# Kernel optimization log

Hardware: AMD Instinct MI355X
Metric: run time of the kernel (lower is better)

The kernel has to match this reference:

```python
import jax, jax.numpy as jnp
import numpy as np

B, T, FEATS, HEAD = 2, 2048, 2048, 16
DIM_HEAD = FEATS // HEAD
EPS = float(jnp.finfo(jnp.float32).eps)  # torch nn.RMSNorm default eps=None -> dtype eps


def _rms_norm(u, g):
    # u: [..., d]; torch RMSNorm: u / sqrt(mean(u^2) + eps) * g
    return u * jax.lax.rsqrt(jnp.mean(u * u, axis=-1, keepdims=True) + EPS) * g


def setup_inputs() -> dict:
    key = jax.random.key(0)
    kx, kw = jax.random.split(key)
    x = jax.random.normal(kx, (B, T, FEATS), dtype=jnp.float32)
    W = jax.random.normal(kw, (FEATS, FEATS), dtype=jnp.float32) / np.sqrt(FEATS)
    g1 = jnp.ones((DIM_HEAD,), dtype=jnp.float32)
    g2 = jnp.ones((DIM_HEAD,), dtype=jnp.float32)
    g3 = jnp.ones((DIM_HEAD,), dtype=jnp.float32)
    return {"x": x, "W": W, "g1": g1, "g2": g2, "g3": g3}


def reference(x, W, g1, g2, g3):
    Bb, Tt, C = x.shape
    sqrt_d = jnp.asarray(DIM_HEAD ** 0.5, dtype=x.dtype)
    # tied QKV projection: torch Linear -> x @ W.T ; then split heads -> [B,H,T,D]
    w = (x @ W.T).reshape(Bb, Tt, HEAD, DIM_HEAD).transpose(0, 2, 1, 3)
    q = _rms_norm(w, g1)
    k = _rms_norm(w, g2)
    v = _rms_norm(w, g3)
    att = jnp.einsum("bhid,bhjd->bhij", q, k) / sqrt_d  # [B,H,T,T]
    # symmetric row + column softmax
    score = jax.nn.softmax(att, axis=-1) + jax.nn.softmax(att, axis=-2)
    y = jnp.einsum("bhij,bhjd->bihd", score, v).reshape(Bb, Tt, C)
    # F.linear(y, W.t()) == y @ W  (tied-weight reprojection)
    return y @ W
```

## Files before the change

kernel.cpp:

```cpp
#include <hip/hip_runtime.h>
#include <stdint.h>

#define T_SEQ 2048
#define B_SZ 2
#define N_HEAD 16
#define D_HEAD 128
#define C_DIM 2048
#define M_ROWS (B_SZ*T_SEQ)
#define N_BH (B_SZ*N_HEAD)

typedef _Float16 f16;
typedef f16 f16x8 __attribute__((ext_vector_type(8)));
typedef f16 f16x4 __attribute__((ext_vector_type(4)));
typedef float f32x4 __attribute__((ext_vector_type(4)));

#define MFMA_F16(a,b,c) __builtin_amdgcn_mfma_f32_16x16x32_f16(a,b,c,0,0,0)

#define BAR_LGKM() do { asm volatile("s_waitcnt lgkmcnt(0)" ::: "memory"); \
                        __builtin_amdgcn_s_barrier(); } while (0)
#define BAR_ALL()  do { asm volatile("s_waitcnt vmcnt(0) lgkmcnt(0)" ::: "memory"); \
                        __builtin_amdgcn_s_barrier(); } while (0)

__device__ __forceinline__ float fexp2(float x) {
#if __has_builtin(__builtin_amdgcn_exp2f)
  return __builtin_amdgcn_exp2f(x);
#else
  float r; asm("v_exp_f32 %0, %1" : "=v"(r) : "v"(x)); return r;
#endif
}

__device__ __forceinline__ void gl_lds16(const void* g, void* l) {
  __builtin_amdgcn_global_load_lds(
      (const __attribute__((address_space(1))) unsigned int*)g,
      (__attribute__((address_space(3))) unsigned int*)l, 16, 0, 0);
}

#define MB_SCALE 0.12752924444069595f
#define RMS_EPS  1.1920928955078125e-07f

__global__ void k_prep(const float* __restrict__ W, const float* __restrict__ x,
                       f16* __restrict__ Wb, f16* __restrict__ Wtb,
                       f16* __restrict__ xb) {
  __shared__ float tile[64][65];
  const int lin = blockIdx.x;
  const int t = threadIdx.x;
  if (lin < 1024) {
    const int bx = (lin & 31) * 64;
    const int by = (lin >> 5) * 64;
    const int tc = t & 63, tr4 = t >> 6;
    for (int rr = tr4; rr < 64; rr += 4) {
      float v = W[(size_t)(by + rr) * C_DIM + bx + tc];
      tile[rr][tc] = v;
      Wb[(size_t)(by + rr) * C_DIM + bx + tc] = (f16)v;
    }
    __syncthreads();
    for (int rr = tr4; rr < 64; rr += 4) {
      Wtb[(size_t)(bx + rr) * C_DIM + by + tc] = (f16)tile[tc][rr];
    }
  } else {
    int i = (lin - 1024) * 256 + t;
    const int stride = 2048 * 256;
    const int n4 = (M_ROWS * C_DIM) / 4;
    for (; i < n4; i += stride) {
      f32x4 v = ((const f32x4*)x)[i];
      f16x4 o; o[0]=(f16)v[0]; o[1]=(f16)v[1]; o[2]=(f16)v[2]; o[3]=(f16)v[3];
      ((f16x4*)xb)[i] = o;
    }
  }
}

template<typename OT>
__global__ __launch_bounds__(256, 2)
void k_gemm_bt(const f16* __restrict__ A, const f16* __restrict__ Bm,
               OT* __restrict__ C, int Nd, int Kd) {
  __shared__ __align__(16) f16 As[2][128 * 64];
  __shared__ __align__(16) f16 Bs[2][128 * 64];
  const int tid = threadIdx.x;
  const int lane = tid & 63, wid = tid >> 6;
  const int lr = lane & 15, lkg = lane >> 4;
  const int wr = wid >> 1, wc = wid & 1;
  const int tm = blockIdx.y * 128, tn = blockIdx.x * 128;

  f32x4 acc[4][4];
#pragma unroll
  for (int i = 0; i < 4; ++i)
#pragma unroll
    for (int j = 0; j < 4; ++j) acc[i][j] = (f32x4){0.f, 0.f, 0.f, 0.f};

  const int nkt = Kd >> 6;

  auto stage = [&](int buf, int kt) {
    const int k0 = kt << 6;
    for (int s = 0; s < 4; ++s) {
      const int r0 = (wid * 4 + s) * 8;
      const int r = r0 + (lane >> 3);
      const int lg = ((lane & 7) ^ (r & 7)) << 3;
      gl_lds16(A + (size_t)(tm + r) * Kd + k0 + lg, &As[buf][r0 * 64]);
      gl_lds16(Bm + (size_t)(tn + r) * Kd + k0 + lg, &Bs[buf][r0 * 64]);
    }
  };

  stage(0, 0);
  int cur = 0;
  for (int kt = 0; kt < nkt; ++kt) {
    __syncthreads();
    if (kt + 1 < nkt) stage(cur ^ 1, kt + 1);
#pragma unroll
    for (int kk = 0; kk < 2; ++kk) {
      f16x8 a[4], b[4];
#pragma unroll
      for (int i = 0; i < 4; ++i) {
        const int ra = wr * 64 + i * 16 + lr;
        const int ga = ((kk * 4 + lkg) ^ (ra & 7)) << 3;
        a[i] = *(const f16x8*)&As[cur][ra * 64 + ga];
        const int rb = wc * 64 + i * 16 + lr;
        const int gb = ((kk * 4 + lkg) ^ (rb & 7)) << 3;
        b[i] = *(const f16x8*)&Bs[cur][rb * 64 + gb];
      }
#pragma unroll
      for (int i = 0; i < 4; ++i)
#pragma unroll
        for (int j = 0; j < 4; ++j) acc[i][j] = MFMA_F16(a[i], b[j], acc[i][j]);
    }
    cur ^= 1;
  }
#pragma unroll
  for (int i = 0; i < 4; ++i) {
    const int row0 = tm + wr * 64 + i * 16 + lkg * 4;
#pragma unroll
    for (int j = 0; j < 4; ++j) {
      const int col = tn + wc * 64 + j * 16 + lr;
#pragma unroll
      for (int r = 0; r < 4; ++r)
        C[(size_t)(row0 + r) * Nd + col] = (OT)acc[i][j][r];
    }
  }
}

__global__ __launch_bounds__(256, 2)
void k_gemm_qkv(const f16* __restrict__ A, const f16* __restrict__ Bm,
                const float* __restrict__ g1, const float* __restrict__ g2,
                f16* __restrict__ nb, f16* __restrict__ mb,
                f16* __restrict__ nT) {
  __shared__ __align__(16) char smem[70656];
  f16 (*As)[128 * 64] = (f16(*)[128 * 64])smem;
  f16 (*Bs)[128 * 64] = (f16(*)[128 * 64])(smem + 32768);
  f16* Cs = (f16*)smem;
  float* sc = (float*)(smem + 69632);

  const int tid = threadIdx.x;
  const int lane = tid & 63, wid = tid >> 6;
  const int lr = lane & 15, lkg = lane >> 4;
  const int wr = wid >> 1, wc = wid & 1;
  const int tm = blockIdx.y * 128;
  const int hh = blockIdx.x;
  const int tn = hh * 128;

  f32x4 acc[4][4];
#pragma unroll
  for (int i = 0; i < 4; ++i)
#pragma unroll
    for (int j = 0; j < 4; ++j) acc[i][j] = (f32x4){0.f, 0.f, 0.f, 0.f};

  auto stage = [&](int buf, int kt) {
    const int k0 = kt << 6;
    for (int s = 0; s < 4; ++s) {
      const int r0 = (wid * 4 + s) * 8;
      const int r = r0 + (lane >> 3);
      const int lg = ((lane & 7) ^ (r & 7)) << 3;
      gl_lds16(A + (size_t)(tm + r) * C_DIM + k0 + lg, &As[buf][r0 * 64]);
      gl_lds16(Bm + (size_t)(tn + r) * C_DIM + k0 + lg, &Bs[buf][r0 * 64]);
    }
  };

  stage(0, 0);
  int cur = 0;
  for (int kt = 0; kt < 32; ++kt) {
    __syncthreads();
    if (kt + 1 < 32) stage(cur ^ 1, kt + 1);
#pragma unroll
    for (int kk = 0; kk < 2; ++kk) {
      f16x8 a[4], b[4];
#pragma unroll
      for (int i = 0; i < 4; ++i) {
        const int ra = wr * 64 + i * 16 + lr;
        const int ga = ((kk * 4 + lkg) ^ (ra & 7)) << 3;
        a[i] = *(const f16x8*)&As[cur][ra * 64 + ga];
        const int rb = wc * 64 + i * 16 + lr;
        const int gb = ((kk * 4 + lkg) ^ (rb & 7)) << 3;
        b[i] = *(const f16x8*)&Bs[cur][rb * 64 + gb];
      }
#pragma unroll
      for (int i = 0; i < 4; ++i)
#pragma unroll
        for (int j = 0; j < 4; ++j) acc[i][j] = MFMA_F16(a[i], b[j], acc[i][j]);
    }
    cur ^= 1;
  }
  __syncthreads();

#pragma unroll
  for (int i = 0; i < 4; ++i)
#pragma unroll
    for (int j = 0; j < 4; ++j)
#pragma unroll
      for (int r = 0; r < 4; ++r)
        Cs[(wr * 64 + i * 16 + lkg * 4 + r) * 136 + wc * 64 + j * 16 + lr] =
            (f16)acc[i][j][r];
  __syncthreads();

  const int row = tid >> 1, dh = tid & 1;
  f16x8 v[8];
  float ss = 0.f;
#pragma unroll
  for (int c = 0; c < 8; ++c) {
    v[c] = *(const f16x8*)&Cs[row * 136 + dh * 64 + c * 8];
#pragma unroll
    for (int e = 0; e < 8; ++e) { float f = (float)v[c][e]; ss += f * f; }
  }
  ss += __shfl_xor(ss, 1);
  const float scale = rsqrtf(ss * (1.f / 128.f) + RMS_EPS);
  if (dh == 0) sc[row] = scale;

  const int grow = tm + row;
  const int b = grow >> 11, ts = grow & (T_SEQ - 1);
  const size_t nbase =
      ((size_t)((b * N_HEAD + hh) * T_SEQ + ts)) * 128 + dh * 64;
#pragma unroll
  for (int c = 0; c < 8; ++c) {
    const int d0 = dh * 64 + c * 8;
    f16x8 n8, m8;
#pragma unroll
    for (int e = 0; e < 8; ++e) {
      const float nf = (float)v[c][e] * scale;
      n8[e] = (f16)nf;
      m8[e] = (f16)(nf * g1[d0 + e] * g2[d0 + e] * MB_SCALE);
    }
    *(f16x8*)&nb[nbase + c * 8] = n8;
    *(f16x8*)&mb[nbase + c * 8] = m8;
  }
  __syncthreads();

  const int dcol = tid >> 1, th = tid & 1;
  const size_t tbase =
      ((size_t)((b * N_HEAD + hh) * 128 + dcol)) * T_SEQ + (tm & (T_SEQ - 1)) +
      th * 64;
#pragma unroll
  for (int rr = 0; rr < 8; ++rr) {
    f16x8 o;
#pragma unroll
    for (int e = 0; e < 8; ++e) {
      const int trow = th * 64 + rr * 8 + e;
      o[e] = (f16)((float)Cs[trow * 136 + dcol] * sc[trow]);
    }
    *(f16x8*)&nT[tbase + rr * 8] = o;
  }
}

__global__ __launch_bounds__(256, 3)
void k_stats_tri(const f16* __restrict__ mIn, const f16* __restrict__ nIn,
                 float* __restrict__ Ssum) {
  __shared__ __align__(16) f16 Ns[128 * 128];
  __shared__ float redR[256];
  __shared__ float redC[256];
  const int tid = threadIdx.x, lane = tid & 63, wid = tid >> 6;
  const int lr = lane & 15, lkg = lane >> 4;
  const int wr = wid >> 1, wc = wid & 1;
  int p = blockIdx.x, it = 0, rowlen = 16;
  while (p >= rowlen) { p -= rowlen; ++it; --rowlen; }
  const int jt = it + p;
  const int bh = blockIdx.y;
  const f16* mp = mIn + (size_t)bh * T_SEQ * 128;
  const f16* np = nIn + (size_t)bh * T_SEQ * 128;

  f16x8 msr[4][4];
#pragma unroll
  for (int i = 0; i < 4; ++i)
#pragma unroll
    for (int kk = 0; kk < 4; ++kk)
      msr[i][kk] = *(const f16x8*)&mp[(size_t)(it * 128 + wr * 64 + i * 16 + lr) * 128 +
                                      (kk * 4 + lkg) * 8];

#pragma unroll
  for (int s = 0; s < 8; ++s) {
    const int r0 = (wid * 8 + s) * 4;
    const int r = r0 + (lane >> 4);
    const int lg = ((lane & 15) ^ (r & 7)) << 3;
    gl_lds16(np + (size_t)(jt * 128 + r) * 128 + lg, &Ns[r0 * 128]);
  }
  BAR_ALL();

  f32x4 acc[4][4];
#pragma unroll
  for (int i = 0; i < 4; ++i)
#pragma unroll
    for (int j = 0; j < 4; ++j) acc[i][j] = (f32x4){0.f, 0.f, 0.f, 0.f};
#pragma unroll
  for (int kk = 0; kk < 4; ++kk) {
    f16x8 b[4];
#pragma unroll
    for (int j = 0; j < 4; ++j) {
      const int rb = wc * 64 + j * 16 + lr;
      const int gb = ((kk * 4 + lkg) ^ (rb & 7)) << 3;
      b[j] = *(const f16x8*)&Ns[rb * 128 + gb];
    }
#pragma unroll
    for (int i = 0; i < 4; ++i)
#pragma unroll
      for (int j = 0; j < 4; ++j)
        acc[i][j] = MFMA_F16(msr[i][kk], b[j], acc[i][j]);
  }

  float rsum[16], csum[4];
#pragma unroll
  for (int q = 0; q < 16; ++q) rsum[q] = 0.f;
#pragma unroll
  for (int j = 0; j < 4; ++j) csum[j] = 0.f;
#pragma unroll
  for (int i = 0; i < 4; ++i)
#pragma unroll
    for (int j = 0; j < 4; ++j)
#pragma unroll
      for (int r = 0; r < 4; ++r) {
        const float e = fexp2(acc[i][j][r]);
        rsum[i * 4 + r] += e;
        csum[j] += e;
      }
#pragma unroll
  for (int q = 0; q < 16; ++q) {
    float v = rsum[q];
    v += __shfl_xor(v, 1); v += __shfl_xor(v, 2);
    v += __shfl_xor(v, 4); v += __shfl_xor(v, 8);
    rsum[q] = v;
  }
  if (lr == 0) {
#pragma unroll
    for (int q = 0; q < 16; ++q) {
      const int row = wr * 64 + (q >> 2) * 16 + lkg * 4 + (q & 3);
      redR[row * 2 + wc] = rsum[q];
    }
  }
#pragma unroll
  for (int j = 0; j < 4; ++j) {
    float v = csum[j];
    v += __shfl_xor(v, 16); v += __shfl_xor(v, 32);
    csum[j] = v;
  }
  if (lkg == 0) {
#pragma unroll
    for (int j = 0; j < 4; ++j) {
      const int col = wc * 64 + j * 16 + lr;
      redC[col * 2 + wr] = csum[j];
    }
  }
  __syncthreads();
  if (tid < 128) {
    const float rS = redR[tid * 2] + redR[tid * 2 + 1];
    atomicAdd(&Ssum[(size_t)bh * T_SEQ + it * 128 + tid], rS);
    if (it != jt) {
      const float cS = redC[tid * 2] + redC[tid * 2 + 1];
      atomicAdd(&Ssum[(size_t)bh * T_SEQ + jt * 128 + tid], cS);
    }
  }
}

__global__ void k_inv(const float* __restrict__ S, float* __restrict__ alpha) {
  const int i = blockIdx.x * blockDim.x + threadIdx.x;
  f32x4 s = ((const f32x4*)S)[i];
  f32x4 a;
#pragma unroll
  for (int e = 0; e < 4; ++e) a[e] = 1.f / s[e];
  ((f32x4*)alpha)[i] = a;
}

__global__ __launch_bounds__(256, 2)
void k_apply(const f16* __restrict__ mIn, const f16* __restrict__ nIn,
             const f16* __restrict__ nTIn, const float* __restrict__ alpha,
             const float* __restrict__ g3, f16* __restrict__ yb) {
  __shared__ __align__(16) f16 Ns[2][64 * 128];
  __shared__ __align__(16) f16 Nts[2][128 * 64];
  __shared__ __align__(16) f16 Ps[128 * 64];
  const int tid = threadIdx.x, lane = tid & 63, wid = tid >> 6;
  const int lr = lane & 15, lkg = lane >> 4;
  const int wj = wid >> 1;
  const int wi = wid & 1;
  const int lin = blockIdx.x + (blockIdx.y << 4);
  const int swz = ((lin & 7) << 6) + (lin >> 3);
  const int it = swz & 15, bh = swz >> 4;
  const int b = bh >> 4, hh = bh & 15;
  const f16* mp = mIn + (size_t)bh * T_SEQ * 128;
  const f16* np = nIn + (size_t)bh * T_SEQ * 128;
  const f16* ntp = nTIn + (size_t)bh * 128 * T_SEQ;
  const float* al = alpha + (size_t)bh * T_SEQ;

  f16x8 msr[4][4];
#pragma unroll
  for (int ii = 0; ii < 4; ++ii)
#pragma unroll
    for (int kk = 0; kk < 4; ++kk)
      msr[ii][kk] = *(const f16x8*)&mp[(size_t)(it * 128 + wi * 64 + ii * 16 + lr) * 128 +
                                       (kk * 4 + lkg) * 8];

  auto stageN = [&](int buf, int jt) {
#pragma unroll
    for (int s = 0; s < 4; ++s) {
      const int r0 = (wid * 4 + s) * 4;
      const int r = r0 + (lane >> 4);
      const int lg = ((lane & 15) ^ (r & 7)) << 3;
      gl_lds16(np + (size_t)(jt * 64 + r) * 128 + lg, &Ns[buf][r0 * 128]);
    }
  };
  auto stageNT = [&](int buf, int jt) {
#pragma unroll
    for (int s = 0; s < 4; ++s) {
      const int r0 = (wid * 4 + s) * 8;
      const int r = r0 + (lane >> 3);
      const int lg = ((lane & 7) ^ (r & 7)) << 3;
      gl_lds16(ntp + (size_t)r * T_SEQ + jt * 64 + lg, &Nts[buf][r0 * 64]);
    }
  };

  float ai[4];
#pragma unroll
  for (int ii = 0; ii < 4; ++ii) ai[ii] = al[it * 128 + wi * 64 + ii * 16 + lr];

  f32x4 yacc[4][4];
#pragma unroll
  for (int i = 0; i < 4; ++i)
#pragma unroll
    for (int j = 0; j < 4; ++j) yacc[i][j] = (f32x4){0.f, 0.f, 0.f, 0.f};

  stageN(0, 0);
  stageNT(0, 0);
  BAR_ALL();
  int cur = 0;
  for (int jt = 0; jt < 32; ++jt) {
    float aj[8];
#pragma unroll
    for (int jj = 0; jj < 2; ++jj)
#pragma unroll
      for (int r = 0; r < 4; ++r)
        aj[jj * 4 + r] = al[jt * 64 + wj * 32 + jj * 16 + lkg * 4 + r];
    if (jt < 31) { stageN(cur ^ 1, jt + 1); stageNT(cur ^ 1, jt + 1); }

    f32x4 acc[2][4];
#pragma unroll
    for (int i = 0; i < 2; ++i)
#pragma unroll
      for (int j = 0; j < 4; ++j) acc[i][j] = (f32x4){0.f, 0.f, 0.f, 0.f};
#pragma unroll
    for (int kk = 0; kk < 4; ++kk) {
      f16x8 a[2];
#pragma unroll
      for (int jj = 0; jj < 2; ++jj) {
        const int jrow = wj * 32 + jj * 16 + lr;
        a[jj] = *(const f16x8*)&Ns[cur][jrow * 128 + (((kk * 4 + lkg) ^ (jrow & 7)) << 3)];
      }
#pragma unroll
      for (int jj = 0; jj < 2; ++jj)
#pragma unroll
        for (int ii = 0; ii < 4; ++ii)
          acc[jj][ii] = MFMA_F16(a[jj], msr[ii][kk], acc[jj][ii]);
    }

#pragma unroll
    for (int jj = 0; jj < 2; ++jj)
#pragma unroll
      for (int ii = 0; ii < 4; ++ii) {
        f16x4 o;
#pragma unroll
        for (int r = 0; r < 4; ++r) {
          const float p = fexp2(acc[jj][ii][r]) * (ai[ii] + aj[jj * 4 + r]);
          o[r] = (f16)p;
        }
        const int il = wi * 64 + ii * 16 + lr;
        const int jl = wj * 32 + jj * 16 + lkg * 4;
        *(f16x4*)&Ps[il * 64 + (((jl >> 3) ^ (il & 7)) << 3) + (jl & 7)] = o;
      }
    BAR_LGKM();

#pragma unroll
    for (int kk = 0; kk < 2; ++kk) {
      f16x8 a[4], bfr[4];
#pragma unroll
      for (int dd = 0; dd < 4; ++dd) {
        const int drow = wj * 64 + dd * 16 + lr;
        a[dd] = *(const f16x8*)&Nts[cur][drow * 64 + (((kk * 4 + lkg) ^ (drow & 7)) << 3)];
      }
#pragma unroll
      for (int ii = 0; ii < 4; ++ii) {
        const int irow = wi * 64 + ii * 16 + lr;
        bfr[ii] = *(const f16x8*)&Ps[irow * 64 + (((kk * 4 + lkg) ^ (irow & 7)) << 3)];
      }
#pragma unroll
      for (int dd = 0; dd < 4; ++dd)
#pragma unroll
        for (int ii = 0; ii < 4; ++ii)
          yacc[dd][ii] = MFMA_F16(a[dd], bfr[ii], yacc[dd][ii]);
    }
    BAR_ALL();
    cur ^= 1;
  }

#pragma unroll
  for (int dd = 0; dd < 4; ++dd) {
    const int d0 = wj * 64 + dd * 16 + lkg * 4;
    float g3v[4];
#pragma unroll
    for (int r = 0; r < 4; ++r) g3v[r] = g3[d0 + r];
#pragma unroll
    for (int ii = 0; ii < 4; ++ii) {
      const int icol = wi * 64 + ii * 16 + lr;
      const size_t base =
          ((size_t)(b * T_SEQ + it * 128 + icol)) * C_DIM + hh * 128 + d0;
      f16x4 o;
#pragma unroll
      for (int r = 0; r < 4; ++r) o[r] = (f16)(yacc[dd][ii][r] * g3v[r]);
      *(f16x4*)&yb[base] = o;
    }
  }
}

extern "C" void kernel_launch(void* const* d_in, const int* in_sizes, int n_in,
                              void* d_out, int out_size, void* d_ws,
                              size_t ws_size, hipStream_t stream) {
  const float* x = (const float*)d_in[0];
  const float* W = (const float*)d_in[1];
  const float* g1 = (const float*)d_in[2];
  const float* g2 = (const float*)d_in[3];
  const float* g3 = (const float*)d_in[4];
  float* out = (float*)d_out;
  char* ws = (char*)d_ws;

  f16* xb   = (f16*)(ws);
  f16* Wb   = (f16*)(ws + 16777216);
  f16* Wtb  = (f16*)(ws + 25165824);
  f16* nb   = (f16*)(ws + 50331648);
  f16* mb   = (f16*)(ws + 67108864);
  f16* nT   = (f16*)(ws + 83886080);
  f16* yb   = (f16*)(ws + 100663296);
  float* alpha = (float*)(ws + 117440512);
  float* Ssum  = (float*)(ws + 117702656);

  hipMemsetAsync(Ssum, 0, 262144, stream);
  k_prep<<<dim3(3072), 256, 0, stream>>>(W, x, Wb, Wtb, xb);
  k_gemm_qkv<<<dim3(16, 32), 256, 0, stream>>>(xb, Wb, g1, g2, nb, mb, nT);
  k_stats_tri<<<dim3(136, 32), 256, 0, stream>>>(mb, nb, Ssum);
  k_inv<<<dim3(64), 256, 0, stream>>>(Ssum, alpha);
  k_apply<<<dim3(16, 32), 256, 0, stream>>>(mb, nb, nT, alpha, g3, yb);
  k_gemm_bt<float><<<dim3(16, 32), 256, 0, stream>>>(yb, Wtb, out, C_DIM, C_DIM);
}
```

Before: 237.7 us.

## Restructure triangular stats kernel into persistent balanced row strips with double-buffered N tiles

Replaces the one-block-per-triangle-tile stats kernel (136x32 blocks) with 512 blocks. Each block pairs row strip p with strip 15-p over a 64-row half, which balances work at 17 tiles per block. N tiles are double-buffered in LDS so the next tile loads while the current one is computed. Row sums accumulate in registers across the strip and are flushed once, while column sums are still written with atomics, deferred by one iteration. The cost is more LDS per block (two 32KB buffers) and lower occupancy, set to 2 blocks per CU.

```diff
diff --git a/kernel.cpp b/kernel.cpp
--- a/kernel.cpp
+++ b/kernel.cpp
@@ -257,111 +257,134 @@
   }
 }
 
-__global__ __launch_bounds__(256, 3)
-void k_stats_tri(const f16* __restrict__ mIn, const f16* __restrict__ nIn,
-                 float* __restrict__ Ssum) {
-  __shared__ __align__(16) f16 Ns[128 * 128];
-  __shared__ float redR[256];
-  __shared__ float redC[256];
+__global__ __launch_bounds__(256, 2)
+void k_stats_strip(const f16* __restrict__ mIn, const f16* __restrict__ nIn,
+                   float* __restrict__ Ssum) {
+  __shared__ __align__(16) f16 Ns[2][128 * 128];
   const int tid = threadIdx.x, lane = tid & 63, wid = tid >> 6;
   const int lr = lane & 15, lkg = lane >> 4;
   const int wr = wid >> 1, wc = wid & 1;
-  int p = blockIdx.x, it = 0, rowlen = 16;
-  while (p >= rowlen) { p -= rowlen; ++it; --rowlen; }
-  const int jt = it + p;
+  const int p = blockIdx.x >> 1, h = blockIdx.x & 1;
+  const int it1 = p, it2 = 15 - p;
+  const int n1 = 16 - p;
   const int bh = blockIdx.y;
   const f16* mp = mIn + (size_t)bh * T_SEQ * 128;
   const f16* np = nIn + (size_t)bh * T_SEQ * 128;
-
-  f16x8 msr[4][4];
-#pragma unroll
-  for (int i = 0; i < 4; ++i)
-#pragma unroll
-    for (int kk = 0; kk < 4; ++kk)
-      msr[i][kk] = *(const f16x8*)&mp[(size_t)(it * 128 + wr * 64 + i * 16 + lr) * 128 +
-                                      (kk * 4 + lkg) * 8];
-
-#pragma unroll
-  for (int s = 0; s < 8; ++s) {
-    const int r0 = (wid * 8 + s) * 4;
-    const int r = r0 + (lane >> 4);
-    const int lg = ((lane & 15) ^ (r & 7)) << 3;
-    gl_lds16(np + (size_t)(jt * 128 + r) * 128 + lg, &Ns[r0 * 128]);
-  }
+  float* Sp = Ssum + (size_t)bh * T_SEQ;
+
+  f16x8 msrW[2][4];
+  auto loadMsr = [&](int itv) {
+#pragma unroll
+    for (int i = 0; i < 2; ++i)
+#pragma unroll
+      for (int kk = 0; kk < 4; ++kk)
+        msrW[i][kk] = *(const f16x8*)&mp[(size_t)(itv * 128 + h * 64 + wr * 32 +
+                                                  i * 16 + lr) * 128 +
+                                         (kk * 4 + lkg) * 8];
+  };
+  auto stageN = [&](int buf, int jt) {
+#pragma unroll
+    for (int s = 0; s < 8; ++s) {
+      const int r0 = (wid * 8 + s) * 4;
+      const int r = r0 + (lane >> 4);
+      const int lg = ((lane & 15) ^ (r & 7)) << 3;
+      gl_lds16(np + (size_t)(jt * 128 + r) * 128 + lg, &Ns[buf][r0 * 128]);
+    }
+  };
+
+  float rsum[8];
+#pragma unroll
+  for (int q = 0; q < 8; ++q) rsum[q] = 0.f;
+  auto flushRows = [&](int itv) {
+#pragma unroll
+    for (int q = 0; q < 8; ++q) {
+      float v = rsum[q];
+      v += __shfl_xor(v, 1); v += __shfl_xor(v, 2);
+      v += __shfl_xor(v, 4); v += __shfl_xor(v, 8);
+      if (lr == 0) {
+        const int row = itv * 128 + h * 64 + wr * 32 + (q >> 2) * 16 +
+                        lkg * 4 + (q & 3);
+        atomicAdd(&Sp[row], v);
+      }
+      rsum[q] = 0.f;
+    }
+  };
+
+  loadMsr(it1);
+  stageN(0, it1);
   BAR_ALL();
-
-  f32x4 acc[4][4];
-#pragma unroll
-  for (int i = 0; i < 4; ++i)
-#pragma unroll
-    for (int j = 0; j < 4; ++j) acc[i][j] = (f32x4){0.f, 0.f, 0.f, 0.f};
-#pragma unroll
-  for (int kk = 0; kk < 4; ++kk) {
-    f16x8 b[4];
-#pragma unroll
-    for (int j = 0; j < 4; ++j) {
-      const int rb = wc * 64 + j * 16 + lr;
-      const int gb = ((kk * 4 + lkg) ^ (rb & 7)) << 3;
-      b[j] = *(const f16x8*)&Ns[rb * 128 + gb];
-    }
-#pragma unroll
-    for (int i = 0; i < 4; ++i)
+  int cur = 0;
+  float csumP[4];
+  int jtP = -1;
+
+  for (int s = 0; s < 17; ++s) {
+    const int itv = (s < n1) ? it1 : it2;
+    const int jt = (s < n1) ? (it1 + s) : (it2 + (s - n1));
+    if (s + 1 < 17) {
+      const int jn = (s + 1 < n1) ? (it1 + s + 1) : (it2 + (s + 1 - n1));
+      stageN(cur ^ 1, jn);
+    }
+    if (jtP >= 0) {
 #pragma unroll
       for (int j = 0; j < 4; ++j)
-        acc[i][j] = MFMA_F16(msr[i][kk], b[j], acc[i][j]);
-  }
-
-  float rsum[16], csum[4];
-#pragma unroll
-  for (int q = 0; q < 16; ++q) rsum[q] = 0.f;
-#pragma unroll
-  for (int j = 0; j < 4; ++j) csum[j] = 0.f;
-#pragma unroll
-  for (int i = 0; i < 4; ++i)
+        if (lkg == 0)
+          atomicAdd(&Sp[jtP * 128 + wc * 64 + j * 16 + lr], csumP[j]);
+      jtP = -1;
+    }
+    if (s == n1) { loadMsr(it2); flushRows(it1); }
+
+    f32x4 acc[2][4];
+#pragma unroll
+    for (int i = 0; i < 2; ++i)
+#pragma unroll
+      for (int j = 0; j < 4; ++j) acc[i][j] = (f32x4){0.f, 0.f, 0.f, 0.f};
+#pragma unroll
+    for (int kk = 0; kk < 4; ++kk) {
+      f16x8 b[4];
+#pragma unroll
+      for (int j = 0; j < 4; ++j) {
+        const int rb = wc * 64 + j * 16 + lr;
+        const int gb = ((kk * 4 + lkg) ^ (rb & 7)) << 3;
+        b[j] = *(const f16x8*)&Ns[cur][rb * 128 + gb];
+      }
+#pragma unroll
+      for (int i = 0; i < 2; ++i)
+#pragma unroll
+        for (int j = 0; j < 4; ++j)
+          acc[i][j] = MFMA_F16(msrW[i][kk], b[j], acc[i][j]);
+    }
+    float cs[4];
+#pragma unroll
+    for (int j = 0; j < 4; ++j) cs[j] = 0.f;
+#pragma unroll
+    for (int i = 0; i < 2; ++i)
+#pragma unroll
+      for (int j = 0; j < 4; ++j)
+#pragma unroll
+        for (int r = 0; r < 4; ++r) {
+          const float e = fexp2(acc[i][j][r]);
+          rsum[i * 4 + r] += e;
+          cs[j] += e;
+        }
+    if (jt != itv) {
+#pragma unroll
+      for (int j = 0; j < 4; ++j) {
+        float v = cs[j];
+        v += __shfl_xor(v, 16); v += __shfl_xor(v, 32);
+        csumP[j] = v;
+      }
+      jtP = jt;
+    }
+    BAR_ALL();
+    cur ^= 1;
+  }
+  if (jtP >= 0) {
 #pragma unroll
     for (int j = 0; j < 4; ++j)
-#pragma unroll
-      for (int r = 0; r < 4; ++r) {
-        const float e = fexp2(acc[i][j][r]);
-        rsum[i * 4 + r] += e;
-        csum[j] += e;
-      }
-#pragma unroll
-  for (int q = 0; q < 16; ++q) {
-    float v = rsum[q];
-    v += __shfl_xor(v, 1); v += __shfl_xor(v, 2);
-    v += __shfl_xor(v, 4); v += __shfl_xor(v, 8);
-    rsum[q] = v;
-  }
-  if (lr == 0) {
-#pragma unroll
-    for (int q = 0; q < 16; ++q) {
-      const int row = wr * 64 + (q >> 2) * 16 + lkg * 4 + (q & 3);
-      redR[row * 2 + wc] = rsum[q];
-    }
-  }
-#pragma unroll
-  for (int j = 0; j < 4; ++j) {
-    float v = csum[j];
-    v += __shfl_xor(v, 16); v += __shfl_xor(v, 32);
-    csum[j] = v;
-  }
-  if (lkg == 0) {
-#pragma unroll
-    for (int j = 0; j < 4; ++j) {
-      const int col = wc * 64 + j * 16 + lr;
-      redC[col * 2 + wr] = csum[j];
-    }
-  }
-  __syncthreads();
-  if (tid < 128) {
-    const float rS = redR[tid * 2] + redR[tid * 2 + 1];
-    atomicAdd(&Ssum[(size_t)bh * T_SEQ + it * 128 + tid], rS);
-    if (it != jt) {
-      const float cS = redC[tid * 2] + redC[tid * 2 + 1];
-      atomicAdd(&Ssum[(size_t)bh * T_SEQ + jt * 128 + tid], cS);
-    }
-  }
+      if (lkg == 0)
+        atomicAdd(&Sp[jtP * 128 + wc * 64 + j * 16 + lr], csumP[j]);
+  }
+  flushRows(it2);
 }
 
 __global__ void k_inv(const float* __restrict__ S, float* __restrict__ alpha) {
@@ -545,7 +568,7 @@
   hipMemsetAsync(Ssum, 0, 262144, stream);
   k_prep<<<dim3(3072), 256, 0, stream>>>(W, x, Wb, Wtb, xb);
   k_gemm_qkv<<<dim3(16, 32), 256, 0, stream>>>(xb, Wb, g1, g2, nb, mb, nT);
-  k_stats_tri<<<dim3(136, 32), 256, 0, stream>>>(mb, nb, Ssum);
+  k_stats_strip<<<dim3(16, 32), 256, 0, stream>>>(mb, nb, Ssum);
   k_inv<<<dim3(64), 256, 0, stream>>>(Ssum, alpha);
   k_apply<<<dim3(16, 32), 256, 0, stream>>>(mb, nb, nT, alpha, g3, yb);
   k_gemm_bt<float><<<dim3(16, 32), 256, 0, stream>>>(yb, Wtb, out, C_DIM, C_DIM);
```

Result: no change. 240.8 us (+1.3%).
